# Kernel tuning notes

Hardware: AMD Instinct MI355X
Metric: run time of the kernel (lower is better)

Reference implementation:

```python
import jax, jax.numpy as jnp
import numpy as np

N_NODES, N_EDGES, N_GRAPHS = 50000, 800000, 128
D_IN, H1, H2, N_CLASSES = 128, 128, 128, 2
NEG_SLOPE = 0.2  # PyG GATConv default


def setup_inputs() -> dict:
    key = jax.random.key(0)
    ks = jax.random.split(key, 12)
    x = jax.random.normal(ks[0], (N_NODES, D_IN), jnp.float32)
    edge_index = jax.random.randint(ks[1], (2, N_EDGES), 0, N_NODES, jnp.int32)
    batch = jnp.sort(jax.random.randint(ks[2], (N_NODES,), 0, N_GRAPHS, jnp.int32))
    s = 0.05
    return {
        "x": x,
        "W1": jax.random.normal(ks[3], (D_IN, H1), jnp.float32) * s,
        "att_src": jax.random.normal(ks[4], (H1,), jnp.float32) * s,
        "att_dst": jax.random.normal(ks[5], (H1,), jnp.float32) * s,
        "b1": jnp.zeros((H1,), jnp.float32),
        "W2": jax.random.normal(ks[6], (H1, H2), jnp.float32) * s,
        "b2": jnp.zeros((H2,), jnp.float32),
        "Wf": jax.random.normal(ks[7], (H2, N_CLASSES), jnp.float32) * s,
        "bf": jnp.zeros((N_CLASSES,), jnp.float32),
        "edge_index": edge_index,
        "batch": batch,
    }


def _add_self_loops(src, dst, n):
    loop = jnp.arange(n, dtype=src.dtype)
    return jnp.concatenate([src, loop]), jnp.concatenate([dst, loop])


def gat_conv(x, W, att_src, att_dst, bias, src, dst, n):
    h = x @ W  # [N, H1]
    a_src = h @ att_src  # [N]
    a_dst = h @ att_dst  # [N]
    e = a_src[src] + a_dst[dst]  # [E']
    e = jnp.where(e > 0, e, NEG_SLOPE * e)  # leaky_relu
    # softmax over incoming edges of each dst node
    m = jax.ops.segment_max(e, dst, num_segments=n)
    ex = jnp.exp(e - m[dst])
    denom = jax.ops.segment_sum(ex, dst, num_segments=n)
    alpha = ex / denom[dst]  # self loops guarantee denom > 0
    out = jax.ops.segment_sum(alpha[:, None] * h[src], dst, num_segments=n)
    return out + bias


def gcn_conv(x, W, bias, src, dst, n):
    h = x @ W  # [N, H2]
    ones = jnp.ones(src.shape[0], h.dtype)
    deg = jax.ops.segment_sum(ones, dst, num_segments=n)
    dinv = jnp.where(deg > 0, jax.lax.rsqrt(deg), 0.0)
    norm = dinv[src] * dinv[dst]  # [E']
    out = jax.ops.segment_sum(norm[:, None] * h[src], dst, num_segments=n)
    return out + bias


def reference(x, W1, att_src, att_dst, b1, W2, b2, Wf, bf, edge_index, batch):
    n = x.shape[0]
    src, dst = _add_self_loops(edge_index[0], edge_index[1], n)
    h = jax.nn.relu(gat_conv(x, W1, att_src, att_dst, b1, src, dst, n))
    h = jax.nn.relu(gcn_conv(h, W2, b2, src, dst, n))
    # global mean pool over graphs
    sums = jax.ops.segment_sum(h, batch, num_segments=N_GRAPHS)
    cnts = jax.ops.segment_sum(jnp.ones((n,), h.dtype), batch, num_segments=N_GRAPHS)
    rep = sums / jnp.maximum(cnts, 1.0)[:, None]
    return rep @ Wf + bf
```

## Files before the change

### kernel.cpp

```cpp
#include <hip/hip_runtime.h>

#define NN 50000
#define NE 800000
#define EP (NE + NN)
#define NG 128
#define F 128
#define NBE 208
#define EPB 4096
#define NBUCK 196
#define BCAP 6144

typedef __attribute__((ext_vector_type(8))) short short8;
typedef __attribute__((ext_vector_type(4))) float float4v;
typedef __attribute__((ext_vector_type(2))) float float2v;
union U8 { uint4 u; short8 s; };

__device__ inline unsigned int bf16rn(float x) {
    unsigned int u = __float_as_uint(x);
    u += 0x7fffu + ((u >> 16) & 1u);
    return u >> 16;
}
__device__ inline unsigned int pack2(float a, float b) {
    return bf16rn(a) | (bf16rn(b) << 16);
}
__device__ inline void bf8_fma2(float2v* acc, float w, uint4 hv) {
    const float2v wv = {w, w};
    float2v p0, p1, p2, p3;
    p0.x = __uint_as_float(hv.x << 16); p0.y = __uint_as_float(hv.x & 0xffff0000u);
    p1.x = __uint_as_float(hv.y << 16); p1.y = __uint_as_float(hv.y & 0xffff0000u);
    p2.x = __uint_as_float(hv.z << 16); p2.y = __uint_as_float(hv.z & 0xffff0000u);
    p3.x = __uint_as_float(hv.w << 16); p3.y = __uint_as_float(hv.w & 0xffff0000u);
    acc[0] += wv * p0;
    acc[1] += wv * p1;
    acc[2] += wv * p2;
    acc[3] += wv * p3;
}

__global__ void pack_wfrag2(const float* __restrict__ W1, const float* __restrict__ W2,
                            uint4* __restrict__ wf, float* __restrict__ gscr,
                            int* __restrict__ cnt) {
    const int p = blockIdx.x * blockDim.x + threadIdx.x;
    if (p >= 4096) {
        const int t = threadIdx.x;
        for (int i = t; i < NG * 32; i += 256) gscr[i] = 0.f;
        for (int i = t; i < NBUCK; i += 256) cnt[i] = 0;
        return;
    }
    const float* W = (p < 2048) ? W1 : W2;
    const int q = p & 2047;
    const int f = q >> 6, l = q & 63;
    const int kt = f >> 3, nt = f & 7;
    const int rb = kt * 32 + ((l >> 4) << 3);
    const int col = nt * 16 + (l & 15);
    const float* wp = W + (size_t)rb * F + col;
    uint4 pk;
    pk.x = pack2(wp[0],     wp[F]);
    pk.y = pack2(wp[2 * F], wp[3 * F]);
    pk.z = pack2(wp[4 * F], wp[5 * F]);
    pk.w = pack2(wp[6 * F], wp[7 * F]);
    wf[p] = pk;
}

__global__ __launch_bounds__(256) void mfma_gemm(
        const unsigned short* __restrict__ Ab, const float* __restrict__ Af,
        const uint4* __restrict__ wf,
        unsigned short* __restrict__ Cb, int N,
        const float* __restrict__ att_src, const float* __restrict__ att_dst,
        float* __restrict__ asrc, float* __restrict__ adst,
        const float* __restrict__ row_scale) {
    const int t = threadIdx.x;
    const int wave = t >> 6, lane = t & 63;
    const int m0 = blockIdx.x * 64 + wave * 16;
    const int arow = m0 + (lane & 15);
    const int kq = (lane >> 4) << 3;
    U8 a[4];
#pragma unroll
    for (int kt = 0; kt < 4; ++kt) {
        if (arow < N) {
            if (Af) {
                const float* ap = Af + (size_t)arow * F + kt * 32 + kq;
                const float4 f0 = *(const float4*)ap;
                const float4 f1 = *(const float4*)(ap + 4);
                a[kt].u = make_uint4(pack2(f0.x, f0.y), pack2(f0.z, f0.w),
                                     pack2(f1.x, f1.y), pack2(f1.z, f1.w));
            } else {
                a[kt].u = *(const uint4*)(Ab + (size_t)arow * F + kt * 32 + kq);
            }
        } else {
            a[kt].u = make_uint4(0, 0, 0, 0);
        }
    }
    const int ccol = lane & 15;
    const int crow0 = m0 + ((lane >> 4) << 2);
    float rs[4] = {1.f, 1.f, 1.f, 1.f};
    if (row_scale) {
#pragma unroll
        for (int r = 0; r < 4; ++r) {
            const int row = crow0 + r;
            if (row < N) rs[r] = row_scale[row];
        }
    }
    float ps[4] = {}, pd[4] = {};
    for (int nt = 0; nt < 8; nt += 2) {
        float4v acc0 = {0.f, 0.f, 0.f, 0.f}, acc1 = {0.f, 0.f, 0.f, 0.f};
#pragma unroll
        for (int kt = 0; kt < 4; ++kt) {
            U8 b0, b1;
            b0.u = wf[(kt * 8 + nt) * 64 + lane];
            b1.u = wf[(kt * 8 + nt + 1) * 64 + lane];
            acc0 = __builtin_amdgcn_mfma_f32_16x16x32_bf16(a[kt].s, b0.s, acc0, 0, 0, 0);
            acc1 = __builtin_amdgcn_mfma_f32_16x16x32_bf16(a[kt].s, b1.s, acc1, 0, 0, 0);
        }
#pragma unroll
        for (int r = 0; r < 4; ++r) {
            const int row = crow0 + r;
            if (row < N) {
                Cb[(size_t)row * F + nt * 16 + ccol]       = (unsigned short)bf16rn(acc0[r] * rs[r]);
                Cb[(size_t)row * F + (nt + 1) * 16 + ccol] = (unsigned short)bf16rn(acc1[r] * rs[r]);
            }
        }
        if (asrc) {
            const float as0 = att_src[nt * 16 + ccol], as1 = att_src[(nt + 1) * 16 + ccol];
            const float ad0 = att_dst[nt * 16 + ccol], ad1 = att_dst[(nt + 1) * 16 + ccol];
#pragma unroll
            for (int r = 0; r < 4; ++r) {
                ps[r] += acc0[r] * as0 + acc1[r] * as1;
                pd[r] += acc0[r] * ad0 + acc1[r] * ad1;
            }
        }
    }
    if (asrc) {
#pragma unroll
        for (int r = 0; r < 4; ++r) {
            float s = ps[r], d = pd[r];
#pragma unroll
            for (int o = 8; o; o >>= 1) { s += __shfl_xor(s, o); d += __shfl_xor(d, o); }
            const int row = crow0 + r;
            if (ccol == 0 && row < N) { asrc[row] = s; adst[row] = d; }
        }
    }
}

__global__ void count_scatter(const int* __restrict__ ei, int* __restrict__ cur,
                              unsigned int* __restrict__ ebuf) {
    __shared__ int lcnt[NBUCK];
    __shared__ int lbase[NBUCK];
    const int t = threadIdx.x, b = blockIdx.x;
    for (int i = t; i < NBUCK; i += 256) lcnt[i] = 0;
    __syncthreads();
    const int e0 = b * EPB;
    int sarr[EPB / 256], darr[EPB / 256];
#pragma unroll
    for (int i = 0; i < EPB / 256; ++i) {
        const int e = e0 + i * 256 + t;
        int s = 0, d = -1;
        if (e < EP) {
            if (e < NE) { s = ei[e]; d = ei[NE + e]; } else { s = d = e - NE; }
            atomicAdd(&lcnt[d >> 8], 1);
        }
        sarr[i] = s; darr[i] = d;
    }
    __syncthreads();
    for (int i = t; i < NBUCK; i += 256) {
        lbase[i] = atomicAdd(&cur[i], lcnt[i]);
        lcnt[i] = 0;
    }
    __syncthreads();
#pragma unroll
    for (int i = 0; i < EPB / 256; ++i) {
        const int d = darr[i];
        if (d >= 0) {
            const int bk = d >> 8;
            const int p = lbase[bk] + atomicAdd(&lcnt[bk], 1);
            ebuf[(size_t)bk * BCAP + p] = (unsigned int)sarr[i] | ((unsigned int)(d & 255) << 16);
        }
    }
}

__global__ void bucket_sort(const unsigned int* __restrict__ ebuf, const int* __restrict__ cnt,
                            int* __restrict__ row_start, unsigned short* __restrict__ csr16,
                            int* __restrict__ deg, float* __restrict__ dinv) {
    __shared__ unsigned int earr[BCAP];
    __shared__ unsigned short out16[BCAP];
    __shared__ int ecnt[256], epre[256];
    const int t = threadIdx.x, g = blockIdx.x;
    const int m = cnt[g];
    const unsigned int* src = ebuf + (size_t)g * BCAP;
    ecnt[t] = 0;
    __syncthreads();
    for (int i = t; i < m; i += 256) {
        const unsigned int v = src[i];
        earr[i] = v;
        atomicAdd(&ecnt[v >> 16], 1);
    }
    __syncthreads();
    const int v0 = ecnt[t];
    epre[t] = v0;
    __syncthreads();
    for (int o = 1; o < 256; o <<= 1) {
        const int u = (t >= o) ? epre[t - o] : 0;
        __syncthreads();
        epre[t] += u;
        __syncthreads();
    }
    const int my_excl = epre[t] - v0;
    const int n = g * 256 + t;
    if (n < NN) {
        row_start[n] = g * BCAP + my_excl;
        deg[n] = v0;
        dinv[n] = rsqrtf((float)v0);
    }
    ecnt[t] = my_excl;
    __syncthreads();
    for (int i = t; i < m; i += 256) {
        const unsigned int v = earr[i];
        const int p = atomicAdd(&ecnt[v >> 16], 1);
        out16[p] = (unsigned short)(v & 0xffffu);
    }
    __syncthreads();
    unsigned short* dst = csr16 + (size_t)g * BCAP;
    for (int i = t; i < m; i += 256) dst[i] = out16[i];
}

__global__ __launch_bounds__(256) void gat_gather(
        const int* __restrict__ row_start, const int* __restrict__ deg,
        const unsigned short* __restrict__ csr_src,
        const float* __restrict__ asrc, const float* __restrict__ adst,
        const unsigned short* __restrict__ hb, const float* __restrict__ bias,
        unsigned short* __restrict__ out) {
    const int lane = threadIdx.x & 63;
    const int qid  = threadIdx.x >> 4;
    const int n    = blockIdx.x * 16 + qid;
    const int lanesub = lane & 15;
    const int qb   = lane & 48;
    const int qo   = lanesub << 3;
    const int lo = row_start[n], hi = lo + deg[n];
    const float adn = adst[n];
    float den = 0.f;
    float2v acc[4];
#pragma unroll
    for (int i = 0; i < 4; ++i) acc[i] = (float2v){0.f, 0.f};
    for (int base = lo; base < hi; base += 16) {
        const int cnt = min(16, hi - base);
        int sv = 0; float ev = 0.f;
        if (lanesub < cnt) {
            sv = csr_src[base + lanesub];
            float sc = asrc[sv] + adn;
            sc = sc > 0.f ? sc : 0.2f * sc;
            ev = __expf(sc);
        }
        den += ev;
        for (int j = 0; j < cnt; j += 8) {
            int ss[8]; float ww[8]; uint4 hh[8];
#pragma unroll
            for (int k = 0; k < 8; ++k) {
                ss[k] = __shfl(sv, qb + j + k);
                ww[k] = __shfl(ev, qb + j + k);
            }
#pragma unroll
            for (int k = 0; k < 8; ++k)
                hh[k] = *(const uint4*)(hb + (size_t)ss[k] * F + qo);
#pragma unroll
            for (int k = 0; k < 8; ++k) bf8_fma2(acc, ww[k], hh[k]);
        }
    }
#pragma unroll
    for (int o = 8; o; o >>= 1) den += __shfl_xor(den, o);
    const float inv = 1.f / den;
    const float4 b0 = *(const float4*)(bias + qo);
    const float4 b1 = *(const float4*)(bias + qo + 4);
    float v[8];
    v[0] = fmaf(acc[0].x, inv, b0.x); v[1] = fmaf(acc[0].y, inv, b0.y);
    v[2] = fmaf(acc[1].x, inv, b0.z); v[3] = fmaf(acc[1].y, inv, b0.w);
    v[4] = fmaf(acc[2].x, inv, b1.x); v[5] = fmaf(acc[2].y, inv, b1.y);
    v[6] = fmaf(acc[3].x, inv, b1.z); v[7] = fmaf(acc[3].y, inv, b1.w);
#pragma unroll
    for (int i = 0; i < 8; ++i) v[i] = v[i] > 0.f ? v[i] : 0.f;
    uint4 pk;
    pk.x = pack2(v[0], v[1]); pk.y = pack2(v[2], v[3]);
    pk.z = pack2(v[4], v[5]); pk.w = pack2(v[6], v[7]);
    *(uint4*)(out + (size_t)n * F + qo) = pk;
}

__global__ __launch_bounds__(256) void gcn_gather_pool(
        const int* __restrict__ row_start, const int* __restrict__ deg,
        const unsigned short* __restrict__ csr_src,
        const float* __restrict__ dinv, const unsigned short* __restrict__ hb,
        const float* __restrict__ bias, const int* __restrict__ batch,
        const float* __restrict__ Wf, float* __restrict__ gscr) {
    __shared__ int   sg[16];
    __shared__ float sp0[16], sp1[16];
    const int lane = threadIdx.x & 63;
    const int qid  = threadIdx.x >> 4;
    const int n    = blockIdx.x * 16 + qid;
    const int lanesub = lane & 15;
    const int qb   = lane & 48;
    const int qo   = lanesub << 3;
    const int lo = row_start[n], hi = lo + deg[n];
    const float dn = dinv[n];
    float2v acc[4];
#pragma unroll
    for (int i = 0; i < 4; ++i) acc[i] = (float2v){0.f, 0.f};
    for (int base = lo; base < hi; base += 16) {
        const int cnt = min(16, hi - base);
        int sv = 0;
        if (lanesub < cnt) sv = csr_src[base + lanesub];
        for (int j = 0; j < cnt; j += 8) {
            int ss[8]; uint4 hh[8];
#pragma unroll
            for (int k = 0; k < 8; ++k) ss[k] = __shfl(sv, qb + j + k);
#pragma unroll
            for (int k = 0; k < 8; ++k)
                hh[k] = *(const uint4*)(hb + (size_t)ss[k] * F + qo);
#pragma unroll
            for (int k = 0; k < 8; ++k) {
                const float w = (j + k < cnt) ? 1.f : 0.f;
                bf8_fma2(acc, w, hh[k]);
            }
        }
    }
    const float4 b0 = *(const float4*)(bias + qo);
    const float4 b1 = *(const float4*)(bias + qo + 4);
    float v[8];
    v[0] = fmaf(acc[0].x, dn, b0.x); v[1] = fmaf(acc[0].y, dn, b0.y);
    v[2] = fmaf(acc[1].x, dn, b0.z); v[3] = fmaf(acc[1].y, dn, b0.w);
    v[4] = fmaf(acc[2].x, dn, b1.x); v[5] = fmaf(acc[2].y, dn, b1.y);
    v[6] = fmaf(acc[3].x, dn, b1.z); v[7] = fmaf(acc[3].y, dn, b1.w);
#pragma unroll
    for (int i = 0; i < 8; ++i) v[i] = v[i] > 0.f ? v[i] : 0.f;
    const float4 w0 = *(const float4*)(Wf + qo * 2);
    const float4 w1 = *(const float4*)(Wf + qo * 2 + 4);
    const float4 w2 = *(const float4*)(Wf + qo * 2 + 8);
    const float4 w3 = *(const float4*)(Wf + qo * 2 + 12);
    float p0 = v[0]*w0.x + v[1]*w0.z + v[2]*w1.x + v[3]*w1.z +
               v[4]*w2.x + v[5]*w2.z + v[6]*w3.x + v[7]*w3.z;
    float p1 = v[0]*w0.y + v[1]*w0.w + v[2]*w1.y + v[3]*w1.w +
               v[4]*w2.y + v[5]*w2.w + v[6]*w3.y + v[7]*w3.w;
#pragma unroll
    for (int o = 8; o; o >>= 1) { p0 += __shfl_xor(p0, o); p1 += __shfl_xor(p1, o); }
    if (lanesub == 0) { sg[qid] = batch[n]; sp0[qid] = p0; sp1[qid] = p1; }
    __syncthreads();
    if (threadIdx.x == 0) {
#pragma unroll 1
        for (int w = 0; w < 16; ++w) {
            const int g = sg[w];
            if (g < 0) continue;
            float q0 = sp0[w], q1 = sp1[w];
            for (int u = w + 1; u < 16; ++u) {
                if (sg[u] == g) { q0 += sp0[u]; q1 += sp1[u]; sg[u] = -1; }
            }
            atomicAdd(gscr + g * 32,     q0);
            atomicAdd(gscr + g * 32 + 1, q1);
        }
    }
}

__global__ void finalize(const float* __restrict__ gscr, const int* __restrict__ batch,
                         const float* __restrict__ bf, float* __restrict__ out) {
    const int g = threadIdx.x;
    int lo = 0, hi = NN;
    while (lo < hi) { int m = (lo + hi) >> 1; if (batch[m] < g) lo = m + 1; else hi = m; }
    int lo2 = lo, hi2 = NN;
    while (lo2 < hi2) { int m = (lo2 + hi2) >> 1; if (batch[m] < g + 1) lo2 = m + 1; else hi2 = m; }
    const float inv = 1.f / fmaxf((float)(lo2 - lo), 1.f);
    out[g * 2]     = gscr[g * 32]     * inv + bf[0];
    out[g * 2 + 1] = gscr[g * 32 + 1] * inv + bf[1];
}

extern "C" void kernel_launch(void* const* d_in, const int* in_sizes, int n_in,
                              void* d_out, int out_size, void* d_ws, size_t ws_size,
                              hipStream_t stream) {
    const float* x       = (const float*)d_in[0];
    const float* W1      = (const float*)d_in[1];
    const float* att_src = (const float*)d_in[2];
    const float* att_dst = (const float*)d_in[3];
    const float* b1      = (const float*)d_in[4];
    const float* W2      = (const float*)d_in[5];
    const float* b2      = (const float*)d_in[6];
    const float* Wf      = (const float*)d_in[7];
    const float* bf      = (const float*)d_in[8];
    const int*   ei      = (const int*)d_in[9];
    const int*   batch   = (const int*)d_in[10];
    float* out = (float*)d_out;

    unsigned short* h1b  = (unsigned short*)d_ws;
    unsigned short* hgb  = h1b + (size_t)NN * F;
    unsigned short* h2b  = hgb + (size_t)NN * F;
    float* asrc      = (float*)(h2b + (size_t)NN * F);
    float* adst      = asrc + NN;
    float* dinv      = adst + NN;
    float* gscr      = dinv + NN;
    int*   row_start = (int*)(gscr + NG * 32);
    int*   deg       = row_start + NN;
    int*   cnt       = deg + NN;
    unsigned short* csr16 = (unsigned short*)(cnt + NBUCK);
    unsigned int*   ebuf  = (unsigned int*)(csr16 + (size_t)NBUCK * BCAP);
    uint4* wf1       = (uint4*)(ebuf + (size_t)NBUCK * BCAP);
    uint4* wf2       = wf1 + 2048;

    pack_wfrag2<<<17, 256, 0, stream>>>(W1, W2, wf1, gscr, cnt);
    count_scatter<<<NBE, 256, 0, stream>>>(ei, cnt, ebuf);
    bucket_sort<<<NBUCK, 256, 0, stream>>>(ebuf, cnt, row_start, csr16, deg, dinv);

    mfma_gemm<<<(NN + 63) / 64, 256, 0, stream>>>(nullptr, x, wf1, h1b, NN,
                                                  att_src, att_dst, asrc, adst, nullptr);
    gat_gather<<<NN / 16, 256, 0, stream>>>(row_start, deg, csr16, asrc, adst,
                                            h1b, b1, hgb);
    mfma_gemm<<<(NN + 63) / 64, 256, 0, stream>>>(hgb, nullptr, wf2, h2b, NN,
                                                  nullptr, nullptr, nullptr, nullptr, dinv);
    gcn_gather_pool<<<NN / 16, 256, 0, stream>>>(row_start, deg, csr16, dinv, h2b, b2,
                                                 batch, Wf, gscr);
    finalize<<<1, NG, 0, stream>>>(gscr, batch, bf, out);
}
```

Baseline: 202.9 us.

## Fuse GEMM1 with edge scatter and GEMM2 into the GAT gather kernel

The first GEMM and the edge count/scatter kernel are merged into one launch, with blocks split by index so the two independent jobs run side by side. The second GEMM is folded into the GAT gather kernel: each block stages its 16 aggregated rows in LDS and runs MFMA on them directly. This removes two launches and the global write and reread of the intermediate hgb buffer. In exchange, each gather block now does a small 16-row GEMM and reloads the W2 fragments, and it adds a block-wide barrier.

```diff
diff --git a/kernel.cpp b/kernel.cpp
--- a/kernel.cpp
+++ b/kernel.cpp
@@ -9,6 +9,7 @@
 #define EPB 4096
 #define NBUCK 196
 #define BCAP 6144
+#define GB1 782
 
 typedef __attribute__((ext_vector_type(8))) short short8;
 typedef __attribute__((ext_vector_type(4))) float float4v;
@@ -61,45 +62,31 @@
     wf[p] = pk;
 }
 
-__global__ __launch_bounds__(256) void mfma_gemm(
-        const unsigned short* __restrict__ Ab, const float* __restrict__ Af,
-        const uint4* __restrict__ wf,
-        unsigned short* __restrict__ Cb, int N,
+__device__ __forceinline__ void gemm1_body(
+        const float* __restrict__ Af, const uint4* __restrict__ wf,
+        unsigned short* __restrict__ Cb,
         const float* __restrict__ att_src, const float* __restrict__ att_dst,
-        float* __restrict__ asrc, float* __restrict__ adst,
-        const float* __restrict__ row_scale) {
+        float* __restrict__ asrc, float* __restrict__ adst, int bid) {
     const int t = threadIdx.x;
     const int wave = t >> 6, lane = t & 63;
-    const int m0 = blockIdx.x * 64 + wave * 16;
+    const int m0 = bid * 64 + wave * 16;
     const int arow = m0 + (lane & 15);
     const int kq = (lane >> 4) << 3;
     U8 a[4];
 #pragma unroll
     for (int kt = 0; kt < 4; ++kt) {
-        if (arow < N) {
-            if (Af) {
-                const float* ap = Af + (size_t)arow * F + kt * 32 + kq;
-                const float4 f0 = *(const float4*)ap;
-                const float4 f1 = *(const float4*)(ap + 4);
-                a[kt].u = make_uint4(pack2(f0.x, f0.y), pack2(f0.z, f0.w),
-                                     pack2(f1.x, f1.y), pack2(f1.z, f1.w));
-            } else {
-                a[kt].u = *(const uint4*)(Ab + (size_t)arow * F + kt * 32 + kq);
-            }
+        if (arow < NN) {
+            const float* ap = Af + (size_t)arow * F + kt * 32 + kq;
+            const float4 f0 = *(const float4*)ap;
+            const float4 f1 = *(const float4*)(ap + 4);
+            a[kt].u = make_uint4(pack2(f0.x, f0.y), pack2(f0.z, f0.w),
+                                 pack2(f1.x, f1.y), pack2(f1.z, f1.w));
         } else {
             a[kt].u = make_uint4(0, 0, 0, 0);
         }
     }
     const int ccol = lane & 15;
     const int crow0 = m0 + ((lane >> 4) << 2);
-    float rs[4] = {1.f, 1.f, 1.f, 1.f};
-    if (row_scale) {
-#pragma unroll
-        for (int r = 0; r < 4; ++r) {
-            const int row = crow0 + r;
-            if (row < N) rs[r] = row_scale[row];
-        }
-    }
     float ps[4] = {}, pd[4] = {};
     for (int nt = 0; nt < 8; nt += 2) {
         float4v acc0 = {0.f, 0.f, 0.f, 0.f}, acc1 = {0.f, 0.f, 0.f, 0.f};
@@ -114,38 +101,43 @@
 #pragma unroll
         for (int r = 0; r < 4; ++r) {
             const int row = crow0 + r;
-            if (row < N) {
-                Cb[(size_t)row * F + nt * 16 + ccol]       = (unsigned short)bf16rn(acc0[r] * rs[r]);
-                Cb[(size_t)row * F + (nt + 1) * 16 + ccol] = (unsigned short)bf16rn(acc1[r] * rs[r]);
+            if (row < NN) {
+                Cb[(size_t)row * F + nt * 16 + ccol]       = (unsigned short)bf16rn(acc0[r]);
+                Cb[(size_t)row * F + (nt + 1) * 16 + ccol] = (unsigned short)bf16rn(acc1[r]);
             }
         }
-        if (asrc) {
-            const float as0 = att_src[nt * 16 + ccol], as1 = att_src[(nt + 1) * 16 + ccol];
-            const float ad0 = att_dst[nt * 16 + ccol], ad1 = att_dst[(nt + 1) * 16 + ccol];
-#pragma unroll
-            for (int r = 0; r < 4; ++r) {
-                ps[r] += acc0[r] * as0 + acc1[r] * as1;
-                pd[r] += acc0[r] * ad0 + acc1[r] * ad1;
-            }
-        }
-    }
-    if (asrc) {
+        const float as0 = att_src[nt * 16 + ccol], as1 = att_src[(nt + 1) * 16 + ccol];
+        const float ad0 = att_dst[nt * 16 + ccol], ad1 = att_dst[(nt + 1) * 16 + ccol];
 #pragma unroll
         for (int r = 0; r < 4; ++r) {
-            float s = ps[r], d = pd[r];
-#pragma unroll
-            for (int o = 8; o; o >>= 1) { s += __shfl_xor(s, o); d += __shfl_xor(d, o); }
-            const int row = crow0 + r;
-            if (ccol == 0 && row < N) { asrc[row] = s; adst[row] = d; }
-        }
-    }
-}
-
-__global__ void count_scatter(const int* __restrict__ ei, int* __restrict__ cur,
-                              unsigned int* __restrict__ ebuf) {
+            ps[r] += acc0[r] * as0 + acc1[r] * as1;
+            pd[r] += acc0[r] * ad0 + acc1[r] * ad1;
+        }
+    }
+#pragma unroll
+    for (int r = 0; r < 4; ++r) {
+        float s = ps[r], d = pd[r];
+#pragma unroll
+        for (int o = 8; o; o >>= 1) { s += __shfl_xor(s, o); d += __shfl_xor(d, o); }
+        const int row = crow0 + r;
+        if (ccol == 0 && row < NN) { asrc[row] = s; adst[row] = d; }
+    }
+}
+
+__global__ __launch_bounds__(256) void gemm1_count_scatter(
+        const float* __restrict__ x, const uint4* __restrict__ wf1,
+        unsigned short* __restrict__ h1b,
+        const float* __restrict__ att_src, const float* __restrict__ att_dst,
+        float* __restrict__ asrc, float* __restrict__ adst,
+        const int* __restrict__ ei, int* __restrict__ cur,
+        unsigned int* __restrict__ ebuf) {
+    if (blockIdx.x < GB1) {
+        gemm1_body(x, wf1, h1b, att_src, att_dst, asrc, adst, blockIdx.x);
+        return;
+    }
     __shared__ int lcnt[NBUCK];
     __shared__ int lbase[NBUCK];
-    const int t = threadIdx.x, b = blockIdx.x;
+    const int t = threadIdx.x, b = blockIdx.x - GB1;
     for (int i = t; i < NBUCK; i += 256) lcnt[i] = 0;
     __syncthreads();
     const int e0 = b * EPB;
@@ -222,12 +214,14 @@
     for (int i = t; i < m; i += 256) dst[i] = out16[i];
 }
 
-__global__ __launch_bounds__(256) void gat_gather(
+__global__ __launch_bounds__(256) void gat_gemm2(
         const int* __restrict__ row_start, const int* __restrict__ deg,
         const unsigned short* __restrict__ csr_src,
         const float* __restrict__ asrc, const float* __restrict__ adst,
         const unsigned short* __restrict__ hb, const float* __restrict__ bias,
-        unsigned short* __restrict__ out) {
+        const uint4* __restrict__ wf2, const float* __restrict__ dinv,
+        unsigned short* __restrict__ h2b) {
+    __shared__ uint4 ldsA[16][17];
     const int lane = threadIdx.x & 63;
     const int qid  = threadIdx.x >> 4;
     const int n    = blockIdx.x * 16 + qid;
@@ -279,7 +273,32 @@
     uint4 pk;
     pk.x = pack2(v[0], v[1]); pk.y = pack2(v[2], v[3]);
     pk.z = pack2(v[4], v[5]); pk.w = pack2(v[6], v[7]);
-    *(uint4*)(out + (size_t)n * F + qo) = pk;
+    ldsA[qid][lanesub] = pk;
+    __syncthreads();
+    const int wave = threadIdx.x >> 6;
+    U8 a[4];
+#pragma unroll
+    for (int kt = 0; kt < 4; ++kt)
+        a[kt].u = ldsA[lane & 15][kt * 4 + (lane >> 4)];
+    const int nt = wave * 2;
+    float4v acc0 = {0.f, 0.f, 0.f, 0.f}, acc1 = {0.f, 0.f, 0.f, 0.f};
+#pragma unroll
+    for (int kt = 0; kt < 4; ++kt) {
+        U8 b0f, b1f;
+        b0f.u = wf2[(kt * 8 + nt) * 64 + lane];
+        b1f.u = wf2[(kt * 8 + nt + 1) * 64 + lane];
+        acc0 = __builtin_amdgcn_mfma_f32_16x16x32_bf16(a[kt].s, b0f.s, acc0, 0, 0, 0);
+        acc1 = __builtin_amdgcn_mfma_f32_16x16x32_bf16(a[kt].s, b1f.s, acc1, 0, 0, 0);
+    }
+    const int ccol = lane & 15;
+    const int crow0 = (lane >> 4) << 2;
+#pragma unroll
+    for (int r = 0; r < 4; ++r) {
+        const int node = blockIdx.x * 16 + crow0 + r;
+        const float rs = dinv[node];
+        h2b[(size_t)node * F + nt * 16 + ccol]       = (unsigned short)bf16rn(acc0[r] * rs);
+        h2b[(size_t)node * F + (nt + 1) * 16 + ccol] = (unsigned short)bf16rn(acc1[r] * rs);
+    }
 }
 
 __global__ __launch_bounds__(256) void gcn_gather_pool(
@@ -399,15 +418,11 @@
     uint4* wf2       = wf1 + 2048;
 
     pack_wfrag2<<<17, 256, 0, stream>>>(W1, W2, wf1, gscr, cnt);
-    count_scatter<<<NBE, 256, 0, stream>>>(ei, cnt, ebuf);
+    gemm1_count_scatter<<<GB1 + NBE, 256, 0, stream>>>(x, wf1, h1b, att_src, att_dst,
+                                                       asrc, adst, ei, cnt, ebuf);
     bucket_sort<<<NBUCK, 256, 0, stream>>>(ebuf, cnt, row_start, csr16, deg, dinv);
-
-    mfma_gemm<<<(NN + 63) / 64, 256, 0, stream>>>(nullptr, x, wf1, h1b, NN,
-                                                  att_src, att_dst, asrc, adst, nullptr);
-    gat_gather<<<NN / 16, 256, 0, stream>>>(row_start, deg, csr16, asrc, adst,
-                                            h1b, b1, hgb);
-    mfma_gemm<<<(NN + 63) / 64, 256, 0, stream>>>(hgb, nullptr, wf2, h2b, NN,
-                                                  nullptr, nullptr, nullptr, nullptr, dinv);
+    gat_gemm2<<<NN / 16, 256, 0, stream>>>(row_start, deg, csr16, asrc, adst,
+                                           h1b, b1, wf2, dinv, h2b);
     gcn_gather_pool<<<NN / 16, 256, 0, stream>>>(row_start, deg, csr16, dinv, h2b, b2,
                                                  batch, Wf, gscr);
     finalize<<<1, NG, 0, stream>>>(gscr, batch, bf, out);
```

New measurement: 187.5 us. -7.6%, faster.
